# Kernel optimization log

Measured on AMD Instinct MI355X. Metric: run time of the kernel, lower is better.

The kernel has to match this reference:

```python
import jax, jax.numpy as jnp
import numpy as np
import math

B, N, DIM, H, DH = 2, 2048, 768, 12, 64
NUM_BUCKETS, MAX_DIST = 32, 128


def _rel_pos_bucket(n):
    # causal bucketing as in T5RelativePositionBias._relative_position_bucket
    rel = jnp.arange(n)[None, :] - jnp.arange(n)[:, None]          # k_pos - q_pos
    neg = jnp.maximum(-rel, 0)                                     # n = max(-rel, 0)
    max_exact = NUM_BUCKETS // 2
    is_small = neg < max_exact
    val_large = max_exact + (
        jnp.log(jnp.maximum(neg, 1).astype(jnp.float32) / max_exact)
        / math.log(MAX_DIST / max_exact) * (NUM_BUCKETS - max_exact)
    ).astype(jnp.int32)
    val_large = jnp.minimum(val_large, NUM_BUCKETS - 1)
    return jnp.where(is_small, neg, val_large)                     # [n, n] int32


def setup_inputs() -> dict:
    key = jax.random.key(0)
    ks = jax.random.split(key, 6)
    s = DIM ** -0.5
    x = jax.random.normal(ks[0], (B, N, DIM), jnp.float32)
    mask = jnp.ones((B, N), dtype=bool)
    Wq = jax.random.normal(ks[1], (DIM, H * DH), jnp.float32) * s
    Wk = jax.random.normal(ks[2], (DIM, H * DH), jnp.float32) * s
    Wv = jax.random.normal(ks[3], (DIM, H * DH), jnp.float32) * s
    Wo = jax.random.normal(ks[4], (H * DH, DIM), jnp.float32) * s
    rel_emb = jax.random.normal(ks[5], (NUM_BUCKETS, H), jnp.float32) * 0.02
    return {"x": x, "mask": mask, "Wq": Wq, "Wk": Wk, "Wv": Wv, "Wo": Wo, "rel_emb": rel_emb}


def reference(x, mask, Wq, Wk, Wv, Wo, rel_emb):
    b, n, _ = x.shape
    scale = DH ** -0.5
    # projections -> [b, h, n, d]
    q = (x @ Wq).reshape(b, n, H, DH).transpose(0, 2, 1, 3) * scale
    k = (x @ Wk).reshape(b, n, H, DH).transpose(0, 2, 1, 3)
    v = (x @ Wv).reshape(b, n, H, DH).transpose(0, 2, 1, 3)
    sim = jnp.einsum('bhid,bhjd->bhij', q, k)                      # [b, h, n, n]
    # relative position bias, also scaled by dim_head**-0.5
    bias = rel_emb[_rel_pos_bucket(n)]                             # [n, n, h]
    sim = sim + jnp.transpose(bias, (2, 0, 1))[None] * scale
    mask_value = -jnp.finfo(sim.dtype).max
    # key/query padding mask: ~mask[:, None, :, None] masks rows (query dim)
    sim = jnp.where(mask[:, None, :, None], sim, mask_value)
    causal = jnp.triu(jnp.ones((n, n), dtype=bool), 1)
    sim = jnp.where(causal[None, None], mask_value, sim)
    attn = jax.nn.softmax(sim, axis=-1)
    out = jnp.einsum('bhij,bhjd->bhid', attn, v)                   # [b, h, n, d]
    out = out.transpose(0, 2, 1, 3).reshape(b, n, H * DH)
    return out @ Wo
```

## Files before the change

### kernel.cpp

```cpp
#include <hip/hip_runtime.h>
#include <math.h>

#define NSEQ 2048
#define HDIM 768
#define NHEAD 12
#define DHEAD 64
#define CHUNK 6
#define NJOBS 51
#define EXP_C1 1.44269504f
#define EXP_C0 -17.3123405f

typedef __attribute__((ext_vector_type(8))) short short8;
typedef __attribute__((ext_vector_type(4))) float f32x4;

static __device__ __forceinline__ unsigned short f2bf(float x) {
    unsigned int u = __float_as_uint(x);
    unsigned int r = (u + 0x7fffu + ((u >> 16) & 1u)) >> 16;
    return (unsigned short)r;
}
static __device__ __forceinline__ float bf2f(unsigned short u) {
    return __uint_as_float(((unsigned int)u) << 16);
}

#define GLD_LDS16(g, l)                                                  \
    __builtin_amdgcn_global_load_lds(                                    \
        (const __attribute__((address_space(1))) void*)(g),              \
        (__attribute__((address_space(3))) void*)(l), 16, 0, 0)

__global__ __launch_bounds__(256) void prep(const float* __restrict__ X,
                                            const float* __restrict__ Wq,
                                            const float* __restrict__ Wk,
                                            const float* __restrict__ Wv,
                                            const float* __restrict__ Wo,
                                            const float* __restrict__ relemb,
                                            unsigned short* __restrict__ Xb,
                                            unsigned short* __restrict__ Wt,
                                            unsigned short* __restrict__ rbg) {
    __shared__ float tb[64][65];
    const int z = blockIdx.x;
    if (z < 576) {
        const int wsel = z / 144, tt = z % 144;
        const int n0 = (tt % 12) * 64, k0 = (tt / 12) * 64;
        const float* W = (wsel == 0) ? Wq : (wsel == 1) ? Wk : (wsel == 2) ? Wv : Wo;
        const float scale = (wsel == 0) ? 0.125f : 1.0f;
        unsigned short* dst = Wt + (size_t)wsel * HDIM * HDIM;
        const int r = threadIdx.x >> 4;
        const int c4 = (threadIdx.x & 15) * 4;
#pragma unroll
        for (int i = 0; i < 4; i++) {
            int row = i * 16 + r;
            float4 v = *(const float4*)(W + (size_t)(k0 + row) * HDIM + n0 + c4);
            tb[c4 + 0][row] = v.x * scale;
            tb[c4 + 1][row] = v.y * scale;
            tb[c4 + 2][row] = v.z * scale;
            tb[c4 + 3][row] = v.w * scale;
        }
        __syncthreads();
#pragma unroll
        for (int i = 0; i < 4; i++) {
            int row = i * 16 + r;
            ushort4 o;
            o.x = f2bf(tb[row][c4 + 0]);
            o.y = f2bf(tb[row][c4 + 1]);
            o.z = f2bf(tb[row][c4 + 2]);
            o.w = f2bf(tb[row][c4 + 3]);
            *(ushort4*)(dst + (size_t)(n0 + row) * HDIM + k0 + c4) = o;
        }
    } else if (z < 960) {
        int base = (z - 576) * 2048 + threadIdx.x;
#pragma unroll
        for (int u = 0; u < 8; u++) {
            int f = base + u * 256;
            float4 v = ((const float4*)X)[f];
            ushort4 o;
            o.x = f2bf(v.x); o.y = f2bf(v.y); o.z = f2bf(v.z); o.w = f2bf(v.w);
            ((ushort4*)Xb)[f] = o;
        }
    } else {
        int idx = (z - 960) * 256 + threadIdx.x;
        int h = idx >> 11;
        int d = idx & (NSEQ - 1);
        int bucket;
        if (d < 16) {
            bucket = d;
        } else {
            float v = logf((float)d * (1.0f / 16.0f)) * (16.0f / logf(8.0f));
            bucket = 16 + (int)v;
            if (bucket > 31) bucket = 31;
        }
        rbg[h * NSEQ + d] = f2bf(relemb[bucket * NHEAD + h] * 0.125f);
    }
}

template <int MODE, int MT>
__global__ __launch_bounds__(256) void gemm_bt(const unsigned short* __restrict__ A,
                                               const unsigned short* __restrict__ Bt,
                                               void* __restrict__ Cout) {
    __shared__ unsigned short As[(MT * 32) * 32];
    __shared__ unsigned short Bs[128 * 32];

    const int tid = threadIdx.x;
    const int w = tid >> 6, lane = tid & 63;
    const int ln = lane & 15, qd = lane >> 4;
    const int wm = w >> 1, wn = w & 1;

    constexpr int NBX = (MODE == 1) ? 18 : 6;
    constexpr int BYG = (MODE == 1) ? 4 : 8;
    const int bid = blockIdx.x;
    const int xcd = bid & 7;
    const int idx = bid >> 3;
    const int by = xcd * BYG + idx / NBX;
    const int bx = idx % NBX;

    const int mat = bx / (HDIM / 128);
    const int n0 = (bx % (HDIM / 128)) * 128;
    const int m0 = by * (MT * 32);
    const unsigned short* Bm = Bt + (size_t)mat * HDIM * HDIM;

    const int scol = (lane & 3) * 8;
    const int arow = w * (MT * 8) + (lane >> 2);
    const int brow = w * 32 + (lane >> 2);
    const unsigned short* agp = A + (size_t)(m0 + arow) * HDIM + scol;
    const unsigned short* bgp = Bm + (size_t)(n0 + brow) * HDIM + scol;
    unsigned short* al = As + (w * (MT * 8)) * 32;
    unsigned short* bl = Bs + (w * 32) * 32;

    f32x4 acc[MT][4];
#pragma unroll
    for (int i = 0; i < MT; i++)
#pragma unroll
        for (int j = 0; j < 4; j++) acc[i][j] = (f32x4){0.f, 0.f, 0.f, 0.f};

    for (int k0 = 0; k0 < HDIM; k0 += 32) {
        __syncthreads();
        GLD_LDS16(agp + k0, al);
        if (MT == 4) GLD_LDS16(agp + 16 * HDIM + k0, al + 16 * 32);
        GLD_LDS16(bgp + k0, bl);
        GLD_LDS16(bgp + 16 * HDIM + k0, bl + 16 * 32);
        __syncthreads();

        short8 af[MT], bf[4];
#pragma unroll
        for (int mt = 0; mt < MT; mt++)
            af[mt] = *(const short8*)&As[(wm * (MT * 16) + mt * 16 + ln) * 32 + qd * 8];
#pragma unroll
        for (int nt = 0; nt < 4; nt++)
            bf[nt] = *(const short8*)&Bs[(wn * 64 + nt * 16 + ln) * 32 + qd * 8];
#pragma unroll
        for (int mt = 0; mt < MT; mt++)
#pragma unroll
            for (int nt = 0; nt < 4; nt++)
                acc[mt][nt] = __builtin_amdgcn_mfma_f32_16x16x32_bf16(
                    af[mt], bf[nt], acc[mt][nt], 0, 0, 0);
    }

    if constexpr (MODE == 0) {
        float* C = (float*)Cout;
#pragma unroll
        for (int mt = 0; mt < MT; mt++)
#pragma unroll
            for (int r = 0; r < 4; r++) {
                int m = m0 + wm * (MT * 16) + mt * 16 + qd * 4 + r;
#pragma unroll
                for (int nt = 0; nt < 4; nt++) {
                    int n = n0 + wn * 64 + nt * 16 + ln;
                    C[(size_t)m * HDIM + n] = acc[mt][nt][r];
                }
            }
    } else {
        const size_t QKVE = (size_t)2 * NHEAD * NSEQ * DHEAD;
        unsigned short* dstm = (unsigned short*)Cout + (size_t)mat * QKVE;
#pragma unroll
        for (int mt = 0; mt < MT; mt++)
#pragma unroll
            for (int r = 0; r < 4; r++) {
                int m = m0 + wm * (MT * 16) + mt * 16 + qd * 4 + r;
                int b = m >> 11, tok = m & (NSEQ - 1);
#pragma unroll
                for (int nt = 0; nt < 4; nt++) {
                    int col = n0 + wn * 64 + nt * 16 + ln;
                    int h = col >> 6, dh = col & 63;
                    dstm[((size_t)(b * NHEAD + h) * NSEQ + tok) * DHEAD + dh] =
                        f2bf(acc[mt][nt][r]);
                }
            }
    }
}

__global__ __launch_bounds__(256) void vtrans(const unsigned short* __restrict__ Vn,
                                              unsigned short* __restrict__ Vt) {
    __shared__ unsigned short Ls[64 * 66];
    const int tid = threadIdx.x;
    const int tok0 = blockIdx.x * 64;
    const size_t bh = blockIdx.y;
    const unsigned short* src = Vn + (bh * NSEQ + tok0) * DHEAD;
    unsigned short* dst = Vt + bh * DHEAD * NSEQ + tok0;

    const int rr = tid >> 3, cc = (tid & 7) * 8;
#pragma unroll
    for (int u = 0; u < 2; u++)
        *(short8*)&Ls[(u * 32 + rr) * 66 + cc] =
            *(const short8*)(src + (size_t)(u * 32 + rr) * DHEAD + cc);
    __syncthreads();
#pragma unroll
    for (int u = 0; u < 2; u++) {
        int dhr = u * 32 + rr;
        short8 v;
#pragma unroll
        for (int e = 0; e < 8; e++) v[e] = Ls[(cc + e) * 66 + dhr];
        *(short8*)(dst + (size_t)dhr * NSEQ + cc) = v;
    }
}

__global__ __launch_bounds__(256) void attn_mfma(const unsigned short* __restrict__ Q,
                                                 const unsigned short* __restrict__ K,
                                                 const unsigned short* __restrict__ Vt_g,
                                                 const unsigned short* __restrict__ rbg,
                                                 unsigned short* __restrict__ AO,
                                                 unsigned short* __restrict__ Of,
                                                 float* __restrict__ Pl) {
    __shared__ __align__(16) unsigned short Ks[64 * 72];
    __shared__ __align__(16) unsigned short Vt[64 * 72];
    __shared__ __align__(16) unsigned short Ps[4 * 32 * 72];
    __shared__ __align__(16) float rbf[512];

    const int tid = threadIdx.x;
    const int w = tid >> 6;
    const int lane = tid & 63;
    const int ln = lane & 15;
    const int qd = lane >> 4;

    const int bid = blockIdx.x;
    const int xcd = bid & 7;
    const int slot = bid >> 3;
    const int bhl = xcd * 3 + slot / NJOBS;
    const int job = NJOBS - 1 - (slot % NJOBS);
    const int b = bhl / NHEAD;
    const int h = bhl - b * NHEAD;

    int qt = 0, cb = 0;
    for (;;) {
        int c = (2 * qt + 2 + CHUNK - 1) / CHUNK;
        if (job < cb + c) break;
        cb += c;
        qt++;
    }
    const int c = (2 * qt + 2 + CHUNK - 1) / CHUNK;
    const int jd = job - cb;
    const int ntk = 2 * qt + 2;
    const int t0 = ntk * jd / c, t1 = ntk * (jd + 1) / c;
    const int i0 = qt * 128;

    const size_t bh = (size_t)bhl;
    const unsigned short* Kb = K + bh * NSEQ * DHEAD;
    const unsigned short* Vg = Vt_g + bh * DHEAD * NSEQ;

    const int wbase = i0 - t1 * 64 + 1;
#pragma unroll
    for (int u = 0; u < 2; u++) {
        int idx = u * 256 + tid;
        int d = wbase + idx;
        int dc = d < 0 ? 0 : (d > NSEQ - 1 ? NSEQ - 1 : d);
        rbf[idx] = (d < 0) ? -1e30f
                           : __fmaf_rn(bf2f(rbg[h * NSEQ + dc]), EXP_C1, EXP_C0);
    }

    short8 qf[2][2];
#pragma unroll
    for (int rg = 0; rg < 2; rg++) {
        const unsigned short* qrow =
            Q + (bh * NSEQ + i0 + w * 32 + rg * 16 + ln) * DHEAD;
        qf[rg][0] = *(const short8*)(qrow + qd * 8);
        qf[rg][1] = *(const short8*)(qrow + 32 + qd * 8);
    }

    short8 ones;
#pragma unroll
    for (int e = 0; e < 8; e++) ones[e] = (short)0x3F80;

    f32x4 o[2][4];
#pragma unroll
    for (int rg = 0; rg < 2; rg++)
#pragma unroll
        for (int cc = 0; cc < 4; cc++) o[rg][cc] = (f32x4){0.f, 0.f, 0.f, 0.f};
    f32x4 o4[2] = {{0.f, 0.f, 0.f, 0.f}, {0.f, 0.f, 0.f, 0.f}};

    int bqs[2];
#pragma unroll
    for (int rg = 0; rg < 2; rg++)
        bqs[rg] = i0 + w * 32 + rg * 16 + ln - qd * 4 - wbase;

    unsigned short* Pw = Ps + w * 32 * 72;

    const int sr = tid >> 3;
    const int sc = (tid & 7) * 8;
    short8 kp[2], vp[2];
    {
        const int jb = t0 * 64;
#pragma unroll
        for (int u = 0; u < 2; u++) {
            kp[u] = *(const short8*)(Kb + (size_t)(jb + u * 32 + sr) * DHEAD + sc);
            vp[u] = *(const short8*)(Vg + (size_t)(u * 32 + sr) * NSEQ + jb + sc);
        }
    }

    for (int t = t0; t < t1; t++) {
        const int jt = t * 64;
        __syncthreads();
#pragma unroll
        for (int u = 0; u < 2; u++) {
            *(short8*)&Ks[(u * 32 + sr) * 72 + sc] = kp[u];
            *(short8*)&Vt[(u * 32 + sr) * 72 + sc] = vp[u];
        }
        __syncthreads();
        if (t + 1 < t1) {
            const int jn = jt + 64;
#pragma unroll
            for (int u = 0; u < 2; u++) {
                kp[u] = *(const short8*)(Kb + (size_t)(jn + u * 32 + sr) * DHEAD + sc);
                vp[u] = *(const short8*)(Vg + (size_t)(u * 32 + sr) * NSEQ + jn + sc);
            }
        }

        short8 kf[4][2];
#pragma unroll
        for (int cc = 0; cc < 4; cc++) {
            kf[cc][0] = *(const short8*)&Ks[(cc * 16 + ln) * 72 + qd * 8];
            kf[cc][1] = *(const short8*)&Ks[(cc * 16 + ln) * 72 + 32 + qd * 8];
        }

#pragma unroll
        for (int rg = 0; rg < 2; rg++) {
            f32x4 st[4] = {{0.f, 0.f, 0.f, 0.f}, {0.f, 0.f, 0.f, 0.f},
                           {0.f, 0.f, 0.f, 0.f}, {0.f, 0.f, 0.f, 0.f}};
#pragma unroll
            for (int cc = 0; cc < 4; cc++) {
                st[cc] = __builtin_amdgcn_mfma_f32_16x16x32_bf16(kf[cc][0], qf[rg][0],
                                                                st[cc], 0, 0, 0);
                st[cc] = __builtin_amdgcn_mfma_f32_16x16x32_bf16(kf[cc][1], qf[rg][1],
                                                                st[cc], 0, 0, 0);
            }
#pragma unroll
            for (int cc = 0; cc < 4; cc++) {
                const int ib = bqs[rg] - jt - cc * 16;
                ushort4 pk;
                pk.x = f2bf(__builtin_amdgcn_exp2f(
                    __fmaf_rn(st[cc][0], EXP_C1, rbf[ib - 0])));
                pk.y = f2bf(__builtin_amdgcn_exp2f(
                    __fmaf_rn(st[cc][1], EXP_C1, rbf[ib - 1])));
                pk.z = f2bf(__builtin_amdgcn_exp2f(
                    __fmaf_rn(st[cc][2], EXP_C1, rbf[ib - 2])));
                pk.w = f2bf(__builtin_amdgcn_exp2f(
                    __fmaf_rn(st[cc][3], EXP_C1, rbf[ib - 3])));
                *(ushort4*)(Pw + (rg * 16 + ln) * 72 + cc * 16 + qd * 4) = pk;
            }
        }

        short8 vf[4][2];
#pragma unroll
        for (int cc = 0; cc < 4; cc++) {
            vf[cc][0] = *(const short8*)&Vt[(cc * 16 + ln) * 72 + qd * 8];
            vf[cc][1] = *(const short8*)&Vt[(cc * 16 + ln) * 72 + 32 + qd * 8];
        }

#pragma unroll
        for (int rg = 0; rg < 2; rg++) {
            short8 pa0 = *(const short8*)(Pw + (rg * 16 + ln) * 72 + qd * 8);
            short8 pa1 = *(const short8*)(Pw + (rg * 16 + ln) * 72 + 32 + qd * 8);
#pragma unroll
            for (int cc = 0; cc < 4; cc++) {
                o[rg][cc] = __builtin_amdgcn_mfma_f32_16x16x32_bf16(pa0, vf[cc][0],
                                                                    o[rg][cc], 0, 0, 0);
                o[rg][cc] = __builtin_amdgcn_mfma_f32_16x16x32_bf16(pa1, vf[cc][1],
                                                                    o[rg][cc], 0, 0, 0);
            }
            o4[rg] = __builtin_amdgcn_mfma_f32_16x16x32_bf16(pa0, ones, o4[rg], 0, 0, 0);
            o4[rg] = __builtin_amdgcn_mfma_f32_16x16x32_bf16(pa1, ones, o4[rg], 0, 0, 0);
        }
    }

    if (job < 3) {
#pragma unroll
        for (int rg = 0; rg < 2; rg++) {
            unsigned short* aop = AO +
                ((size_t)(b * NSEQ) + i0 + w * 32 + rg * 16 + qd * 4) * HDIM +
                h * DHEAD + ln;
#pragma unroll
            for (int r = 0; r < 4; r++) {
                float inv = 1.0f / o4[rg][r];
#pragma unroll
                for (int cc = 0; cc < 4; cc++)
                    aop[(size_t)r * HDIM + cc * 16] = f2bf(o[rg][cc][r] * inv);
            }
        }
    } else {
        const size_t gc = (size_t)bhl * NJOBS + job;
#pragma unroll
        for (int rg = 0; rg < 2; rg++) {
            const int rowl = w * 32 + rg * 16 + qd * 4;
            unsigned short* po = Of + (gc * 128 + rowl) * 64 + ln;
#pragma unroll
            for (int r = 0; r < 4; r++) {
                float inv = 1.0f / o4[rg][r];
#pragma unroll
                for (int cc = 0; cc < 4; cc++)
                    po[(size_t)r * 64 + cc * 16] = f2bf(o[rg][cc][r] * inv);
            }
            if (ln == 0) {
#pragma unroll
                for (int r = 0; r < 4; r++) Pl[gc * 128 + rowl + r] = o4[rg][r];
            }
        }
    }
}

__global__ __launch_bounds__(256) void attn_merge(const unsigned short* __restrict__ Of,
                                                  const float* __restrict__ Pl,
                                                  unsigned short* __restrict__ AO) {
    const int tid = threadIdx.x;
    const int row_g = blockIdx.x * 4 + (tid >> 6);
    const int dh = tid & 63;
    const int bhl = row_g / (NSEQ - 384);
    const int tok = 384 + row_g % (NSEQ - 384);
    const int b = bhl / NHEAD, h = bhl % NHEAD;
    const int g2 = tok >> 7;

    int cb = 0;
    for (int qq = 0; qq < g2; qq++) cb += (2 * qq + 2 + CHUNK - 1) / CHUNK;
    const int c = (2 * g2 + 2 + CHUNK - 1) / CHUNK;
    const int rowl = tok & 127;

    float acc = 0.f, W = 0.f;
    for (int i = 0; i < c; i++) {
        size_t gc = (size_t)bhl * NJOBS + cb + i;
        float l = Pl[gc * 128 + rowl];
        acc += l * bf2f(Of[(gc * 128 + rowl) * 64 + dh]);
        W += l;
    }
    AO[((size_t)(b * NSEQ) + tok) * HDIM + h * DHEAD + dh] = f2bf(acc / W);
}

extern "C" void kernel_launch(void* const* d_in, const int* in_sizes, int n_in,
                              void* d_out, int out_size, void* d_ws, size_t ws_size,
                              hipStream_t stream) {
    const float* x      = (const float*)d_in[0];
    const float* Wq     = (const float*)d_in[2];
    const float* Wk     = (const float*)d_in[3];
    const float* Wv     = (const float*)d_in[4];
    const float* Wo     = (const float*)d_in[5];
    const float* relemb = (const float*)d_in[6];
    float* out = (float*)d_out;

    const size_t QKV = (size_t)2 * NHEAD * NSEQ * DHEAD;
    const size_t NCHUNK = (size_t)24 * NJOBS;
    unsigned short* q   = (unsigned short*)d_ws;
    unsigned short* k   = q + QKV;
    unsigned short* v   = k + QKV;
    unsigned short* vT  = v + QKV;
    unsigned short* aob = vT + QKV;
    unsigned short* xb  = aob + QKV;
    unsigned short* wt  = xb + QKV;
    unsigned short* rbg = wt + (size_t)4 * HDIM * HDIM;
    unsigned short* Of  = rbg + (size_t)NHEAD * NSEQ;
    float* Pl = (float*)(Of + NCHUNK * 128 * 64);

    prep<<<1056, 256, 0, stream>>>(x, Wq, Wk, Wv, Wo, relemb, xb, wt, rbg);

    gemm_bt<1, 4><<<576, 256, 0, stream>>>(xb, wt, q);

    vtrans<<<dim3(NSEQ / 64, 2 * NHEAD), 256, 0, stream>>>(v, vT);

    attn_mfma<<<dim3(8 * 3 * NJOBS), 256, 0, stream>>>(q, k, vT, rbg, aob, Of, Pl);

    attn_merge<<<(24 * (NSEQ - 384)) / 4, 256, 0, stream>>>(Of, Pl, aob);

    gemm_bt<0, 2><<<384, 256, 0, stream>>>(aob, wt + (size_t)3 * HDIM * HDIM, out);
}
```

Before: 169.9 us.

## Fuse x bf16 conversion into QKV GEMM and enlarge attention split chunks

The separate pass that converts x to bf16 is removed; the QKV GEMM now loads fp32 x through registers, converts it, and writes bf16 into LDS, saving one kernel's global traffic. Attention split-K chunking changes from 6 to 8 tiles per chunk (51 to 40 jobs), so more query tiles are handled directly and fewer rows need the merge kernel. The relative-bias LDS buffer grows to cover the wider window, and the GEMM gets a launch-bounds occupancy hint. The register-path A load loses the async global-to-LDS copy and may stall the GEMM main loop.

Measured after the change: 180.1 us. 1.06x slower.

```diff
diff --git a/kernel.cpp b/kernel.cpp
--- a/kernel.cpp
+++ b/kernel.cpp
@@ -5,8 +5,10 @@
 #define HDIM 768
 #define NHEAD 12
 #define DHEAD 64
-#define CHUNK 6
-#define NJOBS 51
+#define CHUNK 8
+#define NJOBS 40
+#define DIRTOK 512
+#define RBFSZ 768
 #define EXP_C1 1.44269504f
 #define EXP_C0 -17.3123405f
 
@@ -27,13 +29,11 @@
         (const __attribute__((address_space(1))) void*)(g),              \
         (__attribute__((address_space(3))) void*)(l), 16, 0, 0)
 
-__global__ __launch_bounds__(256) void prep(const float* __restrict__ X,
-                                            const float* __restrict__ Wq,
+__global__ __launch_bounds__(256) void prep(const float* __restrict__ Wq,
                                             const float* __restrict__ Wk,
                                             const float* __restrict__ Wv,
                                             const float* __restrict__ Wo,
                                             const float* __restrict__ relemb,
-                                            unsigned short* __restrict__ Xb,
                                             unsigned short* __restrict__ Wt,
                                             unsigned short* __restrict__ rbg) {
     __shared__ float tb[64][65];
@@ -66,18 +66,8 @@
             o.w = f2bf(tb[row][c4 + 3]);
             *(ushort4*)(dst + (size_t)(n0 + row) * HDIM + k0 + c4) = o;
         }
-    } else if (z < 960) {
-        int base = (z - 576) * 2048 + threadIdx.x;
-#pragma unroll
-        for (int u = 0; u < 8; u++) {
-            int f = base + u * 256;
-            float4 v = ((const float4*)X)[f];
-            ushort4 o;
-            o.x = f2bf(v.x); o.y = f2bf(v.y); o.z = f2bf(v.z); o.w = f2bf(v.w);
-            ((ushort4*)Xb)[f] = o;
-        }
     } else {
-        int idx = (z - 960) * 256 + threadIdx.x;
+        int idx = (z - 576) * 256 + threadIdx.x;
         int h = idx >> 11;
         int d = idx & (NSEQ - 1);
         int bucket;
@@ -93,9 +83,9 @@
 }
 
 template <int MODE, int MT>
-__global__ __launch_bounds__(256) void gemm_bt(const unsigned short* __restrict__ A,
-                                               const unsigned short* __restrict__ Bt,
-                                               void* __restrict__ Cout) {
+__global__ __launch_bounds__(256, 4) void gemm_bt(const void* __restrict__ Ain,
+                                                  const unsigned short* __restrict__ Bt,
+                                                  void* __restrict__ Cout) {
     __shared__ unsigned short As[(MT * 32) * 32];
     __shared__ unsigned short Bs[128 * 32];
 
@@ -120,10 +110,14 @@
     const int scol = (lane & 3) * 8;
     const int arow = w * (MT * 8) + (lane >> 2);
     const int brow = w * 32 + (lane >> 2);
-    const unsigned short* agp = A + (size_t)(m0 + arow) * HDIM + scol;
     const unsigned short* bgp = Bm + (size_t)(n0 + brow) * HDIM + scol;
+    unsigned short* bl = Bs + (w * 32) * 32;
+
+    const float* Axf = (const float*)Ain;
+    const unsigned short* Axh = (const unsigned short*)Ain;
+    const float* agf = Axf + (size_t)(m0 + arow) * HDIM + scol;
+    const unsigned short* agh = Axh + (size_t)(m0 + arow) * HDIM + scol;
     unsigned short* al = As + (w * (MT * 8)) * 32;
-    unsigned short* bl = Bs + (w * 32) * 32;
 
     f32x4 acc[MT][4];
 #pragma unroll
@@ -133,8 +127,22 @@
 
     for (int k0 = 0; k0 < HDIM; k0 += 32) {
         __syncthreads();
-        GLD_LDS16(agp + k0, al);
-        if (MT == 4) GLD_LDS16(agp + 16 * HDIM + k0, al + 16 * 32);
+        if constexpr (MODE == 1) {
+#pragma unroll
+            for (int rr2 = 0; rr2 < 2; rr2++) {
+                const float* src = agf + (size_t)rr2 * 16 * HDIM + k0;
+                float4 v0 = *(const float4*)(src);
+                float4 v1 = *(const float4*)(src + 4);
+                short8 o;
+                o[0] = (short)f2bf(v0.x); o[1] = (short)f2bf(v0.y);
+                o[2] = (short)f2bf(v0.z); o[3] = (short)f2bf(v0.w);
+                o[4] = (short)f2bf(v1.x); o[5] = (short)f2bf(v1.y);
+                o[6] = (short)f2bf(v1.z); o[7] = (short)f2bf(v1.w);
+                *(short8*)&As[(w * (MT * 8) + (lane >> 2) + rr2 * 16) * 32 + scol] = o;
+            }
+        } else {
+            GLD_LDS16(agh + k0, al);
+        }
         GLD_LDS16(bgp + k0, bl);
         GLD_LDS16(bgp + 16 * HDIM + k0, bl + 16 * 32);
         __syncthreads();
@@ -222,7 +230,7 @@
     __shared__ __align__(16) unsigned short Ks[64 * 72];
     __shared__ __align__(16) unsigned short Vt[64 * 72];
     __shared__ __align__(16) unsigned short Ps[4 * 32 * 72];
-    __shared__ __align__(16) float rbf[512];
+    __shared__ __align__(16) float rbf[RBFSZ];
 
     const int tid = threadIdx.x;
     const int w = tid >> 6;
@@ -257,7 +265,7 @@
 
     const int wbase = i0 - t1 * 64 + 1;
 #pragma unroll
-    for (int u = 0; u < 2; u++) {
+    for (int u = 0; u < 3; u++) {
         int idx = u * 256 + tid;
         int d = wbase + idx;
         int dc = d < 0 ? 0 : (d > NSEQ - 1 ? NSEQ - 1 : d);
@@ -379,7 +387,7 @@
         }
     }
 
-    if (job < 3) {
+    if (job < 4) {
 #pragma unroll
         for (int rg = 0; rg < 2; rg++) {
             unsigned short* aop = AO +
@@ -420,8 +428,8 @@
     const int tid = threadIdx.x;
     const int row_g = blockIdx.x * 4 + (tid >> 6);
     const int dh = tid & 63;
-    const int bhl = row_g / (NSEQ - 384);
-    const int tok = 384 + row_g % (NSEQ - 384);
+    const int bhl = row_g / (NSEQ - DIRTOK);
+    const int tok = DIRTOK + row_g % (NSEQ - DIRTOK);
     const int b = bhl / NHEAD, h = bhl % NHEAD;
     const int g2 = tok >> 7;
 
@@ -458,21 +466,21 @@
     unsigned short* v   = k + QKV;
     unsigned short* vT  = v + QKV;
     unsigned short* aob = vT + QKV;
-    unsigned short* xb  = aob + QKV;
-    unsigned short* wt  = xb + QKV;
+    unsigned short* wt  = aob + QKV;
     unsigned short* rbg = wt + (size_t)4 * HDIM * HDIM;
     unsigned short* Of  = rbg + (size_t)NHEAD * NSEQ;
     float* Pl = (float*)(Of + NCHUNK * 128 * 64);
 
-    prep<<<1056, 256, 0, stream>>>(x, Wq, Wk, Wv, Wo, relemb, xb, wt, rbg);
-
-    gemm_bt<1, 4><<<576, 256, 0, stream>>>(xb, wt, q);
+    prep<<<672, 256, 0, stream>>>(Wq, Wk, Wv, Wo, relemb, wt, rbg);
+
+    gemm_bt<1, 4><<<576, 256, 0, stream>>>((const void*)x, wt, q);
 
     vtrans<<<dim3(NSEQ / 64, 2 * NHEAD), 256, 0, stream>>>(v, vT);
 
     attn_mfma<<<dim3(8 * 3 * NJOBS), 256, 0, stream>>>(q, k, vT, rbg, aob, Of, Pl);
 
-    attn_merge<<<(24 * (NSEQ - 384)) / 4, 256, 0, stream>>>(Of, Pl, aob);
-
-    gemm_bt<0, 2><<<384, 256, 0, stream>>>(aob, wt + (size_t)3 * HDIM * HDIM, out);
-}
+    attn_merge<<<(24 * (NSEQ - DIRTOK)) / 4, 256, 0, stream>>>(Of, Pl, aob);
+
+    gemm_bt<0, 2><<<384, 256, 0, stream>>>((const void*)aob,
+                                           wt + (size_t)3 * HDIM * HDIM, out);
+}
```
